# Kernel tuning notes

Measured on AMD Instinct MI355X. Metric: run time of the kernel, lower is better.

The kernel has to match this reference:

```python
import jax, jax.numpy as jnp
import numpy as np

B, T, D, H, N = 16, 512, 256, 4, 10
DK = D // H
EPS = 1e-12  # espnet LayerNorm eps


def _pe(t, d):
    # espnet PositionalEncoding table
    pos = np.arange(t, dtype=np.float32)[:, None]
    div = np.exp(np.arange(0, d, 2, dtype=np.float32) * (-np.log(10000.0) / d))
    pe = np.zeros((t, d), dtype=np.float32)
    pe[:, 0::2] = np.sin(pos * div)
    pe[:, 1::2] = np.cos(pos * div)
    return jnp.asarray(pe)


def _ln(x, g, b):
    m = jnp.mean(x, -1, keepdims=True)
    v = jnp.var(x, -1, keepdims=True)
    return (x - m) * jax.lax.rsqrt(v + EPS) * g + b


def _forward(x, x_lengths, lids, Wq, bq, Wk, bk, Wv, bv, Wo, bo, W1, b1, W2, b2, g1, be1, g2, be2, gf, bef):
    b, t, d = x.shape
    pe = _pe(t, d)
    pad = jnp.arange(t)[None, :] < x_lengths[:, None]          # [b,t] non-pad mask
    amask = pad[:, None, None, :]                               # [b,1,1,t] key mask
    onehot = (lids[:, None] == jnp.arange(N)[None, :]).astype(x.dtype)  # [b,N]
    h0 = x * np.float32(np.sqrt(d)) + pe[None]                  # scaled input + pos-enc (shared across experts)
    neg = jnp.finfo(x.dtype).min
    out = jnp.zeros_like(x)
    for z in range(N):  # fixed small set of structurally-distinct experts
        # pre-norm self-attention block
        hn = _ln(h0, g1[z], be1[z])
        q = (hn @ Wq[z] + bq[z]).reshape(b, t, H, DK).transpose(0, 2, 1, 3)
        k_ = (hn @ Wk[z] + bk[z]).reshape(b, t, H, DK).transpose(0, 2, 1, 3)
        v_ = (hn @ Wv[z] + bv[z]).reshape(b, t, H, DK).transpose(0, 2, 1, 3)
        scores = jnp.einsum('bhqd,bhkd->bhqk', q, k_) / np.float32(np.sqrt(DK))
        attn = jax.nn.softmax(jnp.where(amask, scores, neg), axis=-1)
        attn = jnp.where(amask, attn, jnp.zeros((), x.dtype))
        ctx = jnp.einsum('bhqk,bhkd->bhqd', attn, v_).transpose(0, 2, 1, 3).reshape(b, t, d)
        h = h0 + ctx @ Wo[z] + bo[z]
        # pre-norm feed-forward block
        hn2 = _ln(h, g2[z], be2[z])
        h = h + jax.nn.relu(hn2 @ W1[z] + b1[z]) @ W2[z] + b2[z]
        # final after_norm, then one-hot masked combine (== emb_lang sum)
        out = out + onehot[:, z, None, None] * _ln(h, gf[z], bef[z])
    return out


def setup_inputs() -> dict:
    key = jax.random.key(0)
    ks = jax.random.split(key, 12)
    s = np.float32(0.02)
    FF = 4 * D
    return {
        'x': jax.random.normal(ks[0], (B, T, D), jnp.float32),
        'x_lengths': jax.random.randint(ks[1], (B,), T // 2, T + 1),
        'lids': jax.random.randint(ks[2], (B,), 0, N),
        'Wq': jax.random.normal(ks[3], (N, D, D), jnp.float32) * s,
        'bq': jnp.zeros((N, D), jnp.float32),
        'Wk': jax.random.normal(ks[4], (N, D, D), jnp.float32) * s,
        'bk': jnp.zeros((N, D), jnp.float32),
        'Wv': jax.random.normal(ks[5], (N, D, D), jnp.float32) * s,
        'bv': jnp.zeros((N, D), jnp.float32),
        'Wo': jax.random.normal(ks[6], (N, D, D), jnp.float32) * s,
        'bo': jnp.zeros((N, D), jnp.float32),
        'W1': jax.random.normal(ks[7], (N, D, FF), jnp.float32) * s,
        'b1': jnp.zeros((N, FF), jnp.float32),
        'W2': jax.random.normal(ks[8], (N, FF, D), jnp.float32) * s,
        'b2': jnp.zeros((N, D), jnp.float32),
        'g1': jnp.ones((N, D), jnp.float32),
        'be1': jnp.zeros((N, D), jnp.float32),
        'g2': jnp.ones((N, D), jnp.float32),
        'be2': jnp.zeros((N, D), jnp.float32),
        'gf': jnp.ones((N, D), jnp.float32),
        'bef': jnp.zeros((N, D), jnp.float32),
    }


def reference(x, x_lengths, lids, Wq, bq, Wk, bk, Wv, bv, Wo, bo, W1, b1, W2, b2, g1, be1, g2, be2, gf, bef):
    return _forward(x, x_lengths, lids, Wq, bq, Wk, bk, Wv, bv, Wo, bo, W1, b1, W2, b2, g1, be1, g2, be2, gf, bef)
```

## Files before the change

### kernel.cpp

```cpp
#include <hip/hip_runtime.h>

typedef unsigned short u16;
typedef __bf16 bf16x8 __attribute__((ext_vector_type(8)));
typedef float  f32x4  __attribute__((ext_vector_type(4)));
typedef unsigned int   u32x4 __attribute__((ext_vector_type(4)));
typedef unsigned short u16x4 __attribute__((ext_vector_type(4)));

#define DEV __device__ __forceinline__

#define NB   16
#define TT   512
#define DD   256
#define HH   4
#define DKH  64
#define NLANG 10
#define FFD  1024

DEV u16 f2bf(float f) {
  unsigned int u = __builtin_bit_cast(unsigned int, f);
  return (u16)((u + 0x7fffu + ((u >> 16) & 1u)) >> 16);
}

DEV f32x4 zero4() { f32x4 z; z[0]=0.f; z[1]=0.f; z[2]=0.f; z[3]=0.f; return z; }

typedef __attribute__((address_space(1))) const unsigned int g_as1;
typedef __attribute__((address_space(3))) unsigned int l_as3;
DEV void load_lds16(const void* g, void* l) {
  __builtin_amdgcn_global_load_lds((g_as1*)g, (l_as3*)l, 16, 0, 0);
}

DEV bf16x8 lds_frag(const u16* lds, int row, int slot) {
  return *(const bf16x8*)(lds + row * 64 + ((slot ^ (row & 7)) << 3));
}

__global__ __launch_bounds__(256) void pre_kernel(
    const float* __restrict__ Wq, const float* __restrict__ Wk,
    const float* __restrict__ Wv, const float* __restrict__ Wo,
    const float* __restrict__ W1, const float* __restrict__ W2,
    u16* __restrict__ wtq, u16* __restrict__ wtk, u16* __restrict__ wtv,
    u16* __restrict__ wto, u16* __restrict__ wt1, u16* __restrict__ wt2,
    const float* __restrict__ x, float* __restrict__ h0, u16* __restrict__ hn,
    const float* __restrict__ g, const float* __restrict__ be,
    const int* __restrict__ lids) {
  __shared__ u16 tile[32][33];
  const int bx = blockIdx.x;
  if (bx < 7680) {
    const float* src; u16* dst; int R, C, z, r0, c0;
    if (bx < 2560) {
      const int w = bx / 640, rem = bx % 640;
      src = (w == 0) ? Wq : (w == 1) ? Wk : (w == 2) ? Wv : Wo;
      dst = (w == 0) ? wtq : (w == 1) ? wtk : (w == 2) ? wtv : wto;
      R = 256; C = 256; z = rem >> 6;
      const int rc = rem & 63; r0 = (rc >> 3) * 32; c0 = (rc & 7) * 32;
    } else if (bx < 5120) {
      const int rem = bx - 2560; src = W1; dst = wt1; R = 256; C = 1024;
      z = rem >> 8; const int rc = rem & 255; r0 = (rc >> 5) * 32; c0 = (rc & 31) * 32;
    } else {
      const int rem = bx - 5120; src = W2; dst = wt2; R = 1024; C = 256;
      z = rem >> 8; const int rc = rem & 255; r0 = (rc >> 3) * 32; c0 = (rc & 7) * 32;
    }
    bool used = false;
#pragma unroll
    for (int i = 0; i < NB; ++i) used |= (lids[i] == z);
    if (!used) return;
    const float* s = src + (size_t)z * R * C;
    u16* d = dst + (size_t)z * R * C;
    const int tx = threadIdx.x & 31, ty = threadIdx.x >> 5;
#pragma unroll
    for (int rr = 0; rr < 4; ++rr) {
      const int r = ty + rr * 8;
      tile[r][tx] = f2bf(s[(size_t)(r0 + r) * C + c0 + tx]);
    }
    __syncthreads();
#pragma unroll
    for (int rr = 0; rr < 4; ++rr) {
      const int cc = ty + rr * 8;
      d[(size_t)(c0 + cc) * R + r0 + tx] = tile[tx][cc];
    }
  } else {
    const int wave = threadIdx.x >> 6, lane = threadIdx.x & 63;
    const int row = (bx - 7680) * 4 + wave;
    const int b = row >> 9, t = row & 511;
    const int z = lids[b];
    const int c0 = lane * 4;
    const float4 xv = *(const float4*)(x + (size_t)row * DD + c0);
    const float kPE = -9.21034037197618f / 256.0f;
    float div0 = __expf(kPE * (float)c0);
    float div1 = __expf(kPE * (float)(c0 + 2));
    float a0 = div0 * (float)t, a1 = div1 * (float)t;
    float h[4];
    h[0] = xv.x * 16.0f + sinf(a0);
    h[1] = xv.y * 16.0f + cosf(a0);
    h[2] = xv.z * 16.0f + sinf(a1);
    h[3] = xv.w * 16.0f + cosf(a1);
    float s = h[0] + h[1] + h[2] + h[3];
    float ss = h[0]*h[0] + h[1]*h[1] + h[2]*h[2] + h[3]*h[3];
#pragma unroll
    for (int d = 1; d < 64; d <<= 1) { s += __shfl_xor(s, d); ss += __shfl_xor(ss, d); }
    float mean = s * (1.0f / 256.0f);
    float var  = ss * (1.0f / 256.0f) - mean * mean;
    float rstd = rsqrtf(var + 1e-12f);
    *(float4*)(h0 + (size_t)row * DD + c0) = make_float4(h[0], h[1], h[2], h[3]);
    u16x4 o;
#pragma unroll
    for (int j = 0; j < 4; ++j)
      o[j] = f2bf((h[j] - mean) * rstd * g[z * DD + c0 + j] + be[z * DD + c0 + j]);
    *(u16x4*)(hn + (size_t)row * DD + c0) = o;
  }
}

template<int OUTF32>
__global__ __launch_bounds__(256) void ln_kernel(const float* __restrict__ in,
                                                 void* __restrict__ outp,
                                                 const float* __restrict__ g,
                                                 const float* __restrict__ be,
                                                 const int* __restrict__ lids) {
  const int wave = threadIdx.x >> 6, lane = threadIdx.x & 63;
  const int row = blockIdx.x * 4 + wave;
  const int b = row >> 9;
  const int z = lids[b];
  const int c0 = lane * 4;
  const float4 v = *(const float4*)(in + (size_t)row * DD + c0);
  float h[4] = {v.x, v.y, v.z, v.w};
  float s = h[0] + h[1] + h[2] + h[3];
  float ss = h[0]*h[0] + h[1]*h[1] + h[2]*h[2] + h[3]*h[3];
#pragma unroll
  for (int d = 1; d < 64; d <<= 1) { s += __shfl_xor(s, d); ss += __shfl_xor(ss, d); }
  float mean = s * (1.0f / 256.0f);
  float var  = ss * (1.0f / 256.0f) - mean * mean;
  float rstd = rsqrtf(var + 1e-12f);
  if (OUTF32) {
    float4 o;
    o.x = (h[0] - mean) * rstd * g[z * DD + c0 + 0] + be[z * DD + c0 + 0];
    o.y = (h[1] - mean) * rstd * g[z * DD + c0 + 1] + be[z * DD + c0 + 1];
    o.z = (h[2] - mean) * rstd * g[z * DD + c0 + 2] + be[z * DD + c0 + 2];
    o.w = (h[3] - mean) * rstd * g[z * DD + c0 + 3] + be[z * DD + c0 + 3];
    *(float4*)((float*)outp + (size_t)row * DD + c0) = o;
  } else {
    u16x4 o;
#pragma unroll
    for (int j = 0; j < 4; ++j)
      o[j] = f2bf((h[j] - mean) * rstd * g[z * DD + c0 + j] + be[z * DD + c0 + j]);
    *(u16x4*)((u16*)outp + (size_t)row * DD + c0) = o;
  }
}

DEV void gemm_tile(const u16* __restrict__ A, const u16* __restrict__ W, int K,
                   int m0, int n0, u16* Alds, u16* Blds, f32x4 acc[4][4]) {
  const int tid = threadIdx.x;
  const int lane = tid & 63;
  const int wave = tid >> 6;
  const int wm = wave >> 1, wn = wave & 1;
  const int l15 = lane & 15, lhi = lane >> 4;
  const int lr = lane >> 3, lsl = lane & 7;
  const u16* srcA[4]; const u16* srcB[4];
#pragma unroll
  for (int j = 0; j < 4; ++j) {
    const int r = wave * 32 + j * 8 + lr;
    srcA[j] = A + (size_t)(m0 + r) * K + ((lsl ^ (r & 7)) << 3);
    srcB[j] = W + (size_t)(n0 + r) * K + ((lsl ^ (r & 7)) << 3);
  }
  for (int k0 = 0; k0 < K; k0 += 64) {
#pragma unroll
    for (int j = 0; j < 4; ++j) {
      load_lds16(srcA[j] + k0, Alds + (wave * 32 + j * 8) * 64);
      load_lds16(srcB[j] + k0, Blds + (wave * 32 + j * 8) * 64);
    }
    __syncthreads();
#pragma unroll
    for (int ks = 0; ks < 2; ++ks) {
      const int slot = ks * 4 + lhi;
      bf16x8 af[4], bfr[4];
#pragma unroll
      for (int m = 0; m < 4; ++m)
        af[m] = lds_frag(Alds, wm * 64 + m * 16 + l15, slot);
#pragma unroll
      for (int n = 0; n < 4; ++n)
        bfr[n] = lds_frag(Blds, wn * 64 + n * 16 + l15, slot);
#pragma unroll
      for (int m = 0; m < 4; ++m)
#pragma unroll
        for (int n = 0; n < 4; ++n)
          acc[m][n] = __builtin_amdgcn_mfma_f32_16x16x32_bf16(af[m], bfr[n], acc[m][n], 0, 0, 0);
    }
    __syncthreads();
  }
}

template<int EPI>
__global__ __launch_bounds__(256) void gemm_kernel(const u16* __restrict__ A,
                                                   const u16* __restrict__ Wt,
                                                   const float* __restrict__ bias,
                                                   const float* __restrict__ res,
                                                   void* __restrict__ outp,
                                                   const int* __restrict__ lids,
                                                   int N, int K) {
  __shared__ u16 Alds[128 * 64];
  __shared__ u16 Blds[128 * 64];
  const int b = blockIdx.z;
  const int z = lids[b];
  const int m0 = blockIdx.y * 128, n0 = blockIdx.x * 128;
  f32x4 acc[4][4];
#pragma unroll
  for (int i = 0; i < 4; ++i)
#pragma unroll
    for (int j = 0; j < 4; ++j) acc[i][j] = zero4();
  gemm_tile(A + (size_t)b * TT * K, Wt + (size_t)z * N * K, K, m0, n0, Alds, Blds, acc);
  const int lane = threadIdx.x & 63, wave = threadIdx.x >> 6;
  const int wm = wave >> 1, wn = wave & 1;
  const int l15 = lane & 15, lhi = lane >> 4;
  float bvv[4];
#pragma unroll
  for (int n = 0; n < 4; ++n) bvv[n] = bias[(size_t)z * N + n0 + wn * 64 + n * 16 + l15];
#pragma unroll
  for (int m = 0; m < 4; ++m) {
    const int grow = m0 + wm * 64 + m * 16 + lhi * 4;
#pragma unroll
    for (int n = 0; n < 4; ++n) {
      const int gcol = n0 + wn * 64 + n * 16 + l15;
#pragma unroll
      for (int r = 0; r < 4; ++r) {
        float v = acc[m][n][r] + bvv[n];
        size_t idx = (size_t)b * TT * N + (size_t)(grow + r) * N + gcol;
        if (EPI == 1) ((u16*)outp)[idx] = f2bf(v > 0.f ? v : 0.f);
        else ((u16*)outp)[idx] = f2bf(v);
      }
    }
  }
}

__global__ __launch_bounds__(256) void gemm64_kernel(const u16* __restrict__ A,
                                                     const u16* __restrict__ Wt,
                                                     const float* __restrict__ bias,
                                                     const float* __restrict__ res,
                                                     float* __restrict__ outp,
                                                     const int* __restrict__ lids,
                                                     int N, int K) {
  __shared__ u16 Alds[128 * 64];
  __shared__ u16 Blds[64 * 64];
  const int b = blockIdx.z;
  const int z = lids[b];
  const int m0 = blockIdx.y * 128, n0 = blockIdx.x * 64;
  const int tid = threadIdx.x, lane = tid & 63, wave = tid >> 6;
  const int l15 = lane & 15, lhi = lane >> 4;
  const int lr = lane >> 3, lsl = lane & 7;
  const u16* Ab = A + (size_t)b * TT * K;
  const u16* Wb = Wt + (size_t)z * N * K;
  const u16* srcA[4]; const u16* srcB[2];
#pragma unroll
  for (int j = 0; j < 4; ++j) {
    const int r = wave * 32 + j * 8 + lr;
    srcA[j] = Ab + (size_t)(m0 + r) * K + ((lsl ^ (r & 7)) << 3);
  }
#pragma unroll
  for (int j = 0; j < 2; ++j) {
    const int r = wave * 16 + j * 8 + lr;
    srcB[j] = Wb + (size_t)(n0 + r) * K + ((lsl ^ (r & 7)) << 3);
  }
  f32x4 acc[2][4];
#pragma unroll
  for (int i = 0; i < 2; ++i)
#pragma unroll
    for (int j = 0; j < 4; ++j) acc[i][j] = zero4();
  for (int k0 = 0; k0 < K; k0 += 64) {
#pragma unroll
    for (int j = 0; j < 4; ++j)
      load_lds16(srcA[j] + k0, Alds + (wave * 32 + j * 8) * 64);
#pragma unroll
    for (int j = 0; j < 2; ++j)
      load_lds16(srcB[j] + k0, Blds + (wave * 16 + j * 8) * 64);
    __syncthreads();
#pragma unroll
    for (int ks = 0; ks < 2; ++ks) {
      const int slot = ks * 4 + lhi;
      bf16x8 af[2], bfr[4];
#pragma unroll
      for (int m = 0; m < 2; ++m)
        af[m] = lds_frag(Alds, wave * 32 + m * 16 + l15, slot);
#pragma unroll
      for (int n = 0; n < 4; ++n)
        bfr[n] = lds_frag(Blds, n * 16 + l15, slot);
#pragma unroll
      for (int m = 0; m < 2; ++m)
#pragma unroll
        for (int n = 0; n < 4; ++n)
          acc[m][n] = __builtin_amdgcn_mfma_f32_16x16x32_bf16(af[m], bfr[n], acc[m][n], 0, 0, 0);
    }
    __syncthreads();
  }
  float bvv[4];
#pragma unroll
  for (int n = 0; n < 4; ++n) bvv[n] = bias[(size_t)z * N + n0 + n * 16 + l15];
#pragma unroll
  for (int m = 0; m < 2; ++m) {
    const int grow = m0 + wave * 32 + m * 16 + lhi * 4;
#pragma unroll
    for (int n = 0; n < 4; ++n) {
      const int gcol = n0 + n * 16 + l15;
#pragma unroll
      for (int r = 0; r < 4; ++r) {
        size_t idx = (size_t)b * TT * N + (size_t)(grow + r) * N + gcol;
        outp[idx] = res[idx] + acc[m][n][r] + bvv[n];
      }
    }
  }
}

__global__ __launch_bounds__(256) void gemm_qkv(const u16* __restrict__ A,
                                                const u16* __restrict__ wtq,
                                                const u16* __restrict__ wtk,
                                                const u16* __restrict__ wtv,
                                                const float* __restrict__ bq,
                                                const float* __restrict__ bk,
                                                const float* __restrict__ bv,
                                                u16* __restrict__ qo,
                                                u16* __restrict__ ko,
                                                u16* __restrict__ vto,
                                                const int* __restrict__ lids) {
  __shared__ u16 Alds[128 * 64];
  __shared__ u16 Blds[128 * 64];
  const int b = blockIdx.z & 15, which = blockIdx.z >> 4;
  const int z = lids[b];
  const u16* W = (which == 0) ? wtq : (which == 1) ? wtk : wtv;
  const float* bias = (which == 0) ? bq : (which == 1) ? bk : bv;
  const int m0 = blockIdx.y * 128, n0 = blockIdx.x * 128;
  f32x4 acc[4][4];
#pragma unroll
  for (int i = 0; i < 4; ++i)
#pragma unroll
    for (int j = 0; j < 4; ++j) acc[i][j] = zero4();
  gemm_tile(A + (size_t)b * TT * DD, W + (size_t)z * DD * DD, DD, m0, n0, Alds, Blds, acc);
  const int lane = threadIdx.x & 63, wave = threadIdx.x >> 6;
  const int wm = wave >> 1, wn = wave & 1;
  const int l15 = lane & 15, lhi = lane >> 4;
  float bvv[4];
#pragma unroll
  for (int n = 0; n < 4; ++n) bvv[n] = bias[(size_t)z * DD + n0 + wn * 64 + n * 16 + l15];
  if (which < 2) {
    u16* out = (which == 0) ? qo : ko;
#pragma unroll
    for (int m = 0; m < 4; ++m) {
      const int grow = m0 + wm * 64 + m * 16 + lhi * 4;
#pragma unroll
      for (int n = 0; n < 4; ++n) {
        const int gcol = n0 + wn * 64 + n * 16 + l15;
#pragma unroll
        for (int r = 0; r < 4; ++r)
          out[(size_t)b * TT * DD + (size_t)(grow + r) * DD + gcol] = f2bf(acc[m][n][r] + bvv[n]);
      }
    }
  } else {
#pragma unroll
    for (int m = 0; m < 4; ++m) {
      const int grow = m0 + wm * 64 + m * 16 + lhi * 4;
#pragma unroll
      for (int n = 0; n < 4; ++n) {
        const int gcol = n0 + wn * 64 + n * 16 + l15;
        u16x4 pk;
#pragma unroll
        for (int r = 0; r < 4; ++r) pk[r] = f2bf(acc[m][n][r] + bvv[n]);
        *(u16x4*)(vto + (size_t)(b * HH + (gcol >> 6)) * DKH * TT + (size_t)(gcol & 63) * TT + grow) = pk;
      }
    }
  }
}

__global__ __launch_bounds__(512, 4) void attn_kernel(const u16* __restrict__ q,
                                                      const u16* __restrict__ k,
                                                      const u16* __restrict__ vt,
                                                      u16* __restrict__ ctx,
                                                      const int* __restrict__ lens) {
  __shared__ char smem[65536];
  u16* Kbuf = (u16*)smem;
  u16* Pbuf = (u16*)(smem + 32768);
  float* Of = (float*)smem;
  float* Ml = (float*)(smem + 32768);
  float* Ll = (float*)(smem + 32768 + 256);

  const int qt = blockIdx.x, h = blockIdx.y, b = blockIdx.z;
  const int tid = threadIdx.x;
  const int lane = tid & 63, wave = tid >> 6;
  const int grp = wave >> 2, wq = wave & 3;
  const int l15 = lane & 15, lhi = lane >> 4;
  const int len = lens[b];
  const int nt = (len + 127) >> 7;
  const int iters = (nt + 1) >> 1;
  const int qrow0 = qt * 64 + wq * 16;
  const u16* qb = q + (size_t)b * TT * DD + h * DKH;
  const u16* kb = k + (size_t)b * TT * DD + h * DKH;
  const u16* vtb = vt + (size_t)(b * HH + h) * DKH * TT;
  const float SC = 0.125f * 1.4426950408889634f;

  u16* Kg = Kbuf + grp * (128 * 64);
  u16* Pg = Pbuf + grp * (64 * 128);

  bf16x8 qf[2];
#pragma unroll
  for (int ks = 0; ks < 2; ++ks)
    qf[ks] = *(const bf16x8*)(qb + (size_t)(qrow0 + l15) * DD + ks * 32 + lhi * 8);

  auto stage = [&](int t) {
    const int r0w = wq * 32;
#pragma unroll
    for (int j = 0; j < 4; ++j) {
      const int rb = r0w + j * 8;
      const int r = rb + (lane >> 3);
      const int s = (lane & 7) ^ (r & 7);
      load_lds16(kb + (size_t)(t * 128 + r) * DD + s * 8, Kg + rb * 64);
    }
  };

  float m[4] = {-1e30f, -1e30f, -1e30f, -1e30f};
  float l[4] = {0.f, 0.f, 0.f, 0.f};
  f32x4 o[4];
#pragma unroll
  for (int d0 = 0; d0 < 4; ++d0) o[d0] = zero4();

  stage(grp);

  for (int i = 0; i < iters; ++i) {
    __syncthreads();
    const int t = 2 * i + grp;
    const bool active = (t < nt);
    if (active) {
      f32x4 S[8];
#pragma unroll
      for (int nb = 0; nb < 8; ++nb) {
        f32x4 a = zero4();
#pragma unroll
        for (int ks = 0; ks < 2; ++ks) {
          const int row = nb * 16 + l15;
          const int swz = (ks * 64 + lhi * 16) ^ ((row & 7) << 4);
          bf16x8 kf = *(const bf16x8*)(Kg + row * 64 + (swz >> 1));
          a = __builtin_amdgcn_mfma_f32_16x16x32_bf16(qf[ks], kf, a, 0, 0, 0);
        }
        S[nb] = a;
      }
      float tmax[4] = {-1e30f, -1e30f, -1e30f, -1e30f};
#pragma unroll
      for (int nb = 0; nb < 8; ++nb) {
        const int col = t * 128 + nb * 16 + l15;
#pragma unroll
        for (int r = 0; r < 4; ++r) {
          float v = S[nb][r] * SC;
          v = (col < len) ? v : -1e30f;
          S[nb][r] = v;
          tmax[r] = fmaxf(tmax[r], v);
        }
      }
#pragma unroll
      for (int d = 1; d < 16; d <<= 1)
#pragma unroll
        for (int r = 0; r < 4; ++r) tmax[r] = fmaxf(tmax[r], __shfl_xor(tmax[r], d));
      float al[4];
#pragma unroll
      for (int r = 0; r < 4; ++r) {
        float mn = fmaxf(m[r], tmax[r]);
        al[r] = exp2f(m[r] - mn);
        m[r] = mn;
      }
      float rs[4] = {0.f, 0.f, 0.f, 0.f};
#pragma unroll
      for (int nb = 0; nb < 8; ++nb) {
#pragma unroll
        for (int r = 0; r < 4; ++r) {
          float p = exp2f(S[nb][r] - m[r]);
          rs[r] += p;
          const int lrow = wq * 16 + lhi * 4 + r;
          const int swzb = ((nb * 16 + l15) * 2) ^ ((lrow & 7) << 4);
          Pg[(lrow * 256 + swzb) >> 1] = f2bf(p);
        }
      }
#pragma unroll
      for (int d = 1; d < 16; d <<= 1)
#pragma unroll
        for (int r = 0; r < 4; ++r) rs[r] += __shfl_xor(rs[r], d);
#pragma unroll
      for (int r = 0; r < 4; ++r) l[r] = l[r] * al[r] + rs[r];
#pragma unroll
      for (int d0 = 0; d0 < 4; ++d0)
#pragma unroll
        for (int r = 0; r < 4; ++r) o[d0][r] *= al[r];
    }
    __syncthreads();
    if (t + 2 < nt) stage(t + 2);
    if (active) {
      const int arow = wq * 16 + l15;
#pragma unroll
      for (int ks = 0; ks < 4; ++ks) {
        const int swz = (ks * 64 + lhi * 16) ^ ((arow & 7) << 4);
        bf16x8 pf = *(const bf16x8*)(Pg + arow * 128 + (swz >> 1));
#pragma unroll
        for (int d0 = 0; d0 < 4; ++d0) {
          bf16x8 vf = *(const bf16x8*)(vtb + (size_t)(d0 * 16 + l15) * TT + t * 128 + ks * 32 + lhi * 8);
          o[d0] = __builtin_amdgcn_mfma_f32_16x16x32_bf16(pf, vf, o[d0], 0, 0, 0);
        }
      }
    }
  }

  __syncthreads();
  if (grp == 1) {
#pragma unroll
    for (int d0 = 0; d0 < 4; ++d0)
#pragma unroll
      for (int r = 0; r < 4; ++r)
        Of[(wq * 16 + lhi * 4 + r) * 68 + d0 * 16 + l15] = o[d0][r];
    if (l15 == 0) {
#pragma unroll
      for (int r = 0; r < 4; ++r) {
        Ml[wq * 16 + lhi * 4 + r] = m[r];
        Ll[wq * 16 + lhi * 4 + r] = l[r];
      }
    }
  }
  __syncthreads();
  if (grp == 0) {
    u16* cb = ctx + (size_t)b * TT * DD + h * DKH;
#pragma unroll
    for (int r = 0; r < 4; ++r) {
      const int lrow = wq * 16 + lhi * 4 + r;
      const float m1 = Ml[lrow], l1 = Ll[lrow];
      const float mn = fmaxf(m[r], m1);
      const float a0 = exp2f(m[r] - mn), a1 = exp2f(m1 - mn);
      const float linv = 1.0f / (l[r] * a0 + l1 * a1);
#pragma unroll
      for (int d0 = 0; d0 < 4; ++d0) {
        const float of = Of[lrow * 68 + d0 * 16 + l15];
        const float out = (o[d0][r] * a0 + of * a1) * linv;
        cb[(size_t)(qt * 64 + lrow) * DD + d0 * 16 + l15] = f2bf(out);
      }
    }
  }
}

extern "C" void kernel_launch(void* const* d_in, const int* in_sizes, int n_in,
                              void* d_out, int out_size, void* d_ws, size_t ws_size,
                              hipStream_t stream) {
  (void)in_sizes; (void)n_in; (void)out_size; (void)ws_size;
  const float* x    = (const float*)d_in[0];
  const int*   xlen = (const int*)d_in[1];
  const int*   lids = (const int*)d_in[2];
  const float* Wq = (const float*)d_in[3];
  const float* bq = (const float*)d_in[4];
  const float* Wk = (const float*)d_in[5];
  const float* bk = (const float*)d_in[6];
  const float* Wv = (const float*)d_in[7];
  const float* bv = (const float*)d_in[8];
  const float* Wo = (const float*)d_in[9];
  const float* bo = (const float*)d_in[10];
  const float* W1 = (const float*)d_in[11];
  const float* b1 = (const float*)d_in[12];
  const float* W2 = (const float*)d_in[13];
  const float* b2 = (const float*)d_in[14];
  const float* g1 = (const float*)d_in[15];
  const float* be1= (const float*)d_in[16];
  const float* g2 = (const float*)d_in[17];
  const float* be2= (const float*)d_in[18];
  const float* gf = (const float*)d_in[19];
  const float* bef= (const float*)d_in[20];

  char* ws = (char*)d_ws;
  size_t off = 0;
  auto alloc = [&](size_t bytes) -> void* {
    void* p = ws + off;
    off = (off + bytes + 255) & ~(size_t)255;
    return p;
  };
  u16* wtq = (u16*)alloc((size_t)NLANG * DD * DD * 2);
  u16* wtk = (u16*)alloc((size_t)NLANG * DD * DD * 2);
  u16* wtv = (u16*)alloc((size_t)NLANG * DD * DD * 2);
  u16* wto = (u16*)alloc((size_t)NLANG * DD * DD * 2);
  u16* wt1 = (u16*)alloc((size_t)NLANG * DD * FFD * 2);
  u16* wt2 = (u16*)alloc((size_t)NLANG * FFD * DD * 2);
  float* h0 = (float*)alloc((size_t)NB * TT * DD * 4);
  float* hc = (float*)alloc((size_t)NB * TT * DD * 4);
  u16* hn  = (u16*)alloc((size_t)NB * TT * DD * 2);
  u16* qb  = (u16*)alloc((size_t)NB * TT * DD * 2);
  u16* kb  = (u16*)alloc((size_t)NB * TT * DD * 2);
  u16* vtb = (u16*)alloc((size_t)NB * TT * DD * 2);
  u16* ctx = (u16*)alloc((size_t)NB * TT * DD * 2);
  u16* ffn = (u16*)alloc((size_t)NB * TT * FFD * 2);

  pre_kernel<<<dim3(7680 + 2048), 256, 0, stream>>>(
      Wq, Wk, Wv, Wo, W1, W2, wtq, wtk, wtv, wto, wt1, wt2,
      x, h0, hn, g1, be1, lids);

  gemm_qkv<<<dim3(2, 4, 48), 256, 0, stream>>>(hn, wtq, wtk, wtv, bq, bk, bv, qb, kb, vtb, lids);

  attn_kernel<<<dim3(8, HH, NB), 512, 0, stream>>>(qb, kb, vtb, ctx, xlen);

  gemm64_kernel<<<dim3(4, 4, NB), 256, 0, stream>>>(ctx, wto, bo, h0, hc, lids, DD, DD);

  ln_kernel<0><<<dim3(NB * TT / 4), 256, 0, stream>>>(hc, hn, g2, be2, lids);

  gemm_kernel<1><<<dim3(8, 4, NB), 256, 0, stream>>>(hn, wt1, b1, nullptr, ffn, lids, FFD, DD);

  gemm64_kernel<<<dim3(4, 4, NB), 256, 0, stream>>>(ffn, wt2, b2, hc, hc, lids, DD, FFD);

  ln_kernel<1><<<dim3(NB * TT / 4), 256, 0, stream>>>(hc, d_out, gf, bef, lids);
}
```

Baseline: 105.2 us.

## Fuse residual-add and LayerNorm into full-row GEMMs; drop K staging in attention

The Wo and W2 projections now run in a new gemm_ln_kernel. Each block computes all 256 output columns for 32 rows, so it can add bias and residual and apply LayerNorm in the epilogue. This removes two standalone LN kernels and a round trip of the fp32 hidden state through memory. The attention kernel drops its LDS double-buffered K staging and block-wide syncs and reads K fragments straight from global memory, with a per-wave P buffer and a flattened grid. In exchange the fused GEMM has only 256 blocks, each reloading the full weight slab, and the K loads in attention are now uncoalesced global reads.

```diff
diff --git a/kernel.cpp b/kernel.cpp
--- a/kernel.cpp
+++ b/kernel.cpp
@@ -109,42 +109,6 @@
   }
 }
 
-template<int OUTF32>
-__global__ __launch_bounds__(256) void ln_kernel(const float* __restrict__ in,
-                                                 void* __restrict__ outp,
-                                                 const float* __restrict__ g,
-                                                 const float* __restrict__ be,
-                                                 const int* __restrict__ lids) {
-  const int wave = threadIdx.x >> 6, lane = threadIdx.x & 63;
-  const int row = blockIdx.x * 4 + wave;
-  const int b = row >> 9;
-  const int z = lids[b];
-  const int c0 = lane * 4;
-  const float4 v = *(const float4*)(in + (size_t)row * DD + c0);
-  float h[4] = {v.x, v.y, v.z, v.w};
-  float s = h[0] + h[1] + h[2] + h[3];
-  float ss = h[0]*h[0] + h[1]*h[1] + h[2]*h[2] + h[3]*h[3];
-#pragma unroll
-  for (int d = 1; d < 64; d <<= 1) { s += __shfl_xor(s, d); ss += __shfl_xor(ss, d); }
-  float mean = s * (1.0f / 256.0f);
-  float var  = ss * (1.0f / 256.0f) - mean * mean;
-  float rstd = rsqrtf(var + 1e-12f);
-  if (OUTF32) {
-    float4 o;
-    o.x = (h[0] - mean) * rstd * g[z * DD + c0 + 0] + be[z * DD + c0 + 0];
-    o.y = (h[1] - mean) * rstd * g[z * DD + c0 + 1] + be[z * DD + c0 + 1];
-    o.z = (h[2] - mean) * rstd * g[z * DD + c0 + 2] + be[z * DD + c0 + 2];
-    o.w = (h[3] - mean) * rstd * g[z * DD + c0 + 3] + be[z * DD + c0 + 3];
-    *(float4*)((float*)outp + (size_t)row * DD + c0) = o;
-  } else {
-    u16x4 o;
-#pragma unroll
-    for (int j = 0; j < 4; ++j)
-      o[j] = f2bf((h[j] - mean) * rstd * g[z * DD + c0 + j] + be[z * DD + c0 + j]);
-    *(u16x4*)((u16*)outp + (size_t)row * DD + c0) = o;
-  }
-}
-
 DEV void gemm_tile(const u16* __restrict__ A, const u16* __restrict__ W, int K,
                    int m0, int n0, u16* Alds, u16* Blds, f32x4 acc[4][4]) {
   const int tid = threadIdx.x;
@@ -191,7 +155,6 @@
 __global__ __launch_bounds__(256) void gemm_kernel(const u16* __restrict__ A,
                                                    const u16* __restrict__ Wt,
                                                    const float* __restrict__ bias,
-                                                   const float* __restrict__ res,
                                                    void* __restrict__ outp,
                                                    const int* __restrict__ lids,
                                                    int N, int K) {
@@ -224,83 +187,6 @@
         size_t idx = (size_t)b * TT * N + (size_t)(grow + r) * N + gcol;
         if (EPI == 1) ((u16*)outp)[idx] = f2bf(v > 0.f ? v : 0.f);
         else ((u16*)outp)[idx] = f2bf(v);
-      }
-    }
-  }
-}
-
-__global__ __launch_bounds__(256) void gemm64_kernel(const u16* __restrict__ A,
-                                                     const u16* __restrict__ Wt,
-                                                     const float* __restrict__ bias,
-                                                     const float* __restrict__ res,
-                                                     float* __restrict__ outp,
-                                                     const int* __restrict__ lids,
-                                                     int N, int K) {
-  __shared__ u16 Alds[128 * 64];
-  __shared__ u16 Blds[64 * 64];
-  const int b = blockIdx.z;
-  const int z = lids[b];
-  const int m0 = blockIdx.y * 128, n0 = blockIdx.x * 64;
-  const int tid = threadIdx.x, lane = tid & 63, wave = tid >> 6;
-  const int l15 = lane & 15, lhi = lane >> 4;
-  const int lr = lane >> 3, lsl = lane & 7;
-  const u16* Ab = A + (size_t)b * TT * K;
-  const u16* Wb = Wt + (size_t)z * N * K;
-  const u16* srcA[4]; const u16* srcB[2];
-#pragma unroll
-  for (int j = 0; j < 4; ++j) {
-    const int r = wave * 32 + j * 8 + lr;
-    srcA[j] = Ab + (size_t)(m0 + r) * K + ((lsl ^ (r & 7)) << 3);
-  }
-#pragma unroll
-  for (int j = 0; j < 2; ++j) {
-    const int r = wave * 16 + j * 8 + lr;
-    srcB[j] = Wb + (size_t)(n0 + r) * K + ((lsl ^ (r & 7)) << 3);
-  }
-  f32x4 acc[2][4];
-#pragma unroll
-  for (int i = 0; i < 2; ++i)
-#pragma unroll
-    for (int j = 0; j < 4; ++j) acc[i][j] = zero4();
-  for (int k0 = 0; k0 < K; k0 += 64) {
-#pragma unroll
-    for (int j = 0; j < 4; ++j)
-      load_lds16(srcA[j] + k0, Alds + (wave * 32 + j * 8) * 64);
-#pragma unroll
-    for (int j = 0; j < 2; ++j)
-      load_lds16(srcB[j] + k0, Blds + (wave * 16 + j * 8) * 64);
-    __syncthreads();
-#pragma unroll
-    for (int ks = 0; ks < 2; ++ks) {
-      const int slot = ks * 4 + lhi;
-      bf16x8 af[2], bfr[4];
-#pragma unroll
-      for (int m = 0; m < 2; ++m)
-        af[m] = lds_frag(Alds, wave * 32 + m * 16 + l15, slot);
-#pragma unroll
-      for (int n = 0; n < 4; ++n)
-        bfr[n] = lds_frag(Blds, n * 16 + l15, slot);
-#pragma unroll
-      for (int m = 0; m < 2; ++m)
-#pragma unroll
-        for (int n = 0; n < 4; ++n)
-          acc[m][n] = __builtin_amdgcn_mfma_f32_16x16x32_bf16(af[m], bfr[n], acc[m][n], 0, 0, 0);
-    }
-    __syncthreads();
-  }
-  float bvv[4];
-#pragma unroll
-  for (int n = 0; n < 4; ++n) bvv[n] = bias[(size_t)z * N + n0 + n * 16 + l15];
-#pragma unroll
-  for (int m = 0; m < 2; ++m) {
-    const int grow = m0 + wave * 32 + m * 16 + lhi * 4;
-#pragma unroll
-    for (int n = 0; n < 4; ++n) {
-      const int gcol = n0 + n * 16 + l15;
-#pragma unroll
-      for (int r = 0; r < 4; ++r) {
-        size_t idx = (size_t)b * TT * N + (size_t)(grow + r) * N + gcol;
-        outp[idx] = res[idx] + acc[m][n][r] + bvv[n];
       }
     }
   }
@@ -370,45 +256,30 @@
                                                       const u16* __restrict__ vt,
                                                       u16* __restrict__ ctx,
                                                       const int* __restrict__ lens) {
-  __shared__ char smem[65536];
-  u16* Kbuf = (u16*)smem;
-  u16* Pbuf = (u16*)(smem + 32768);
-  float* Of = (float*)smem;
-  float* Ml = (float*)(smem + 32768);
-  float* Ll = (float*)(smem + 32768 + 256);
-
-  const int qt = blockIdx.x, h = blockIdx.y, b = blockIdx.z;
+  __shared__ char smem[33792];
+  const int id = blockIdx.x;
+  const int qt = id >> 6, bh = id & 63, b = bh >> 2, h = bh & 3;
   const int tid = threadIdx.x;
   const int lane = tid & 63, wave = tid >> 6;
   const int grp = wave >> 2, wq = wave & 3;
   const int l15 = lane & 15, lhi = lane >> 4;
   const int len = lens[b];
   const int nt = (len + 127) >> 7;
-  const int iters = (nt + 1) >> 1;
   const int qrow0 = qt * 64 + wq * 16;
   const u16* qb = q + (size_t)b * TT * DD + h * DKH;
   const u16* kb = k + (size_t)b * TT * DD + h * DKH;
   const u16* vtb = vt + (size_t)(b * HH + h) * DKH * TT;
   const float SC = 0.125f * 1.4426950408889634f;
 
-  u16* Kg = Kbuf + grp * (128 * 64);
-  u16* Pg = Pbuf + grp * (64 * 128);
+  u16* Pg = (u16*)(smem + wave * 4096);
+  float* Of = (float*)smem;
+  float* Ml = (float*)(smem + 32768);
+  float* Ll = (float*)(smem + 33024);
 
   bf16x8 qf[2];
 #pragma unroll
   for (int ks = 0; ks < 2; ++ks)
     qf[ks] = *(const bf16x8*)(qb + (size_t)(qrow0 + l15) * DD + ks * 32 + lhi * 8);
-
-  auto stage = [&](int t) {
-    const int r0w = wq * 32;
-#pragma unroll
-    for (int j = 0; j < 4; ++j) {
-      const int rb = r0w + j * 8;
-      const int r = rb + (lane >> 3);
-      const int s = (lane & 7) ^ (r & 7);
-      load_lds16(kb + (size_t)(t * 128 + r) * DD + s * 8, Kg + rb * 64);
-    }
-  };
 
   float m[4] = {-1e30f, -1e30f, -1e30f, -1e30f};
   float l[4] = {0.f, 0.f, 0.f, 0.f};
@@ -416,85 +287,71 @@
 #pragma unroll
   for (int d0 = 0; d0 < 4; ++d0) o[d0] = zero4();
 
-  stage(grp);
-
-  for (int i = 0; i < iters; ++i) {
-    __syncthreads();
-    const int t = 2 * i + grp;
-    const bool active = (t < nt);
-    if (active) {
-      f32x4 S[8];
-#pragma unroll
-      for (int nb = 0; nb < 8; ++nb) {
-        f32x4 a = zero4();
-#pragma unroll
-        for (int ks = 0; ks < 2; ++ks) {
-          const int row = nb * 16 + l15;
-          const int swz = (ks * 64 + lhi * 16) ^ ((row & 7) << 4);
-          bf16x8 kf = *(const bf16x8*)(Kg + row * 64 + (swz >> 1));
-          a = __builtin_amdgcn_mfma_f32_16x16x32_bf16(qf[ks], kf, a, 0, 0, 0);
-        }
-        S[nb] = a;
-      }
-      float tmax[4] = {-1e30f, -1e30f, -1e30f, -1e30f};
-#pragma unroll
-      for (int nb = 0; nb < 8; ++nb) {
-        const int col = t * 128 + nb * 16 + l15;
-#pragma unroll
-        for (int r = 0; r < 4; ++r) {
-          float v = S[nb][r] * SC;
-          v = (col < len) ? v : -1e30f;
-          S[nb][r] = v;
-          tmax[r] = fmaxf(tmax[r], v);
-        }
-      }
-#pragma unroll
-      for (int d = 1; d < 16; d <<= 1)
-#pragma unroll
-        for (int r = 0; r < 4; ++r) tmax[r] = fmaxf(tmax[r], __shfl_xor(tmax[r], d));
-      float al[4];
+  for (int t = grp; t < nt; t += 2) {
+    f32x4 S[8];
+#pragma unroll
+    for (int nb = 0; nb < 8; ++nb) {
+      f32x4 a = zero4();
+#pragma unroll
+      for (int ks = 0; ks < 2; ++ks) {
+        bf16x8 kf = *(const bf16x8*)(kb + (size_t)(t * 128 + nb * 16 + l15) * DD + ks * 32 + lhi * 8);
+        a = __builtin_amdgcn_mfma_f32_16x16x32_bf16(qf[ks], kf, a, 0, 0, 0);
+      }
+      S[nb] = a;
+    }
+    float tmax[4] = {-1e30f, -1e30f, -1e30f, -1e30f};
+#pragma unroll
+    for (int nb = 0; nb < 8; ++nb) {
+      const int col = t * 128 + nb * 16 + l15;
 #pragma unroll
       for (int r = 0; r < 4; ++r) {
-        float mn = fmaxf(m[r], tmax[r]);
-        al[r] = exp2f(m[r] - mn);
-        m[r] = mn;
-      }
-      float rs[4] = {0.f, 0.f, 0.f, 0.f};
-#pragma unroll
-      for (int nb = 0; nb < 8; ++nb) {
-#pragma unroll
-        for (int r = 0; r < 4; ++r) {
-          float p = exp2f(S[nb][r] - m[r]);
-          rs[r] += p;
-          const int lrow = wq * 16 + lhi * 4 + r;
-          const int swzb = ((nb * 16 + l15) * 2) ^ ((lrow & 7) << 4);
-          Pg[(lrow * 256 + swzb) >> 1] = f2bf(p);
-        }
-      }
-#pragma unroll
-      for (int d = 1; d < 16; d <<= 1)
-#pragma unroll
-        for (int r = 0; r < 4; ++r) rs[r] += __shfl_xor(rs[r], d);
-#pragma unroll
-      for (int r = 0; r < 4; ++r) l[r] = l[r] * al[r] + rs[r];
-#pragma unroll
-      for (int d0 = 0; d0 < 4; ++d0)
-#pragma unroll
-        for (int r = 0; r < 4; ++r) o[d0][r] *= al[r];
-    }
-    __syncthreads();
-    if (t + 2 < nt) stage(t + 2);
-    if (active) {
-      const int arow = wq * 16 + l15;
-#pragma unroll
-      for (int ks = 0; ks < 4; ++ks) {
-        const int swz = (ks * 64 + lhi * 16) ^ ((arow & 7) << 4);
-        bf16x8 pf = *(const bf16x8*)(Pg + arow * 128 + (swz >> 1));
-#pragma unroll
-        for (int d0 = 0; d0 < 4; ++d0) {
-          bf16x8 vf = *(const bf16x8*)(vtb + (size_t)(d0 * 16 + l15) * TT + t * 128 + ks * 32 + lhi * 8);
-          o[d0] = __builtin_amdgcn_mfma_f32_16x16x32_bf16(pf, vf, o[d0], 0, 0, 0);
-        }
+        float v = S[nb][r] * SC;
+        v = (col < len) ? v : -1e30f;
+        S[nb][r] = v;
+        tmax[r] = fmaxf(tmax[r], v);
+      }
+    }
+#pragma unroll
+    for (int d = 1; d < 16; d <<= 1)
+#pragma unroll
+      for (int r = 0; r < 4; ++r) tmax[r] = fmaxf(tmax[r], __shfl_xor(tmax[r], d));
+    float al[4];
+#pragma unroll
+    for (int r = 0; r < 4; ++r) {
+      float mn = fmaxf(m[r], tmax[r]);
+      al[r] = exp2f(m[r] - mn);
+      m[r] = mn;
+    }
+    float rs[4] = {0.f, 0.f, 0.f, 0.f};
+#pragma unroll
+    for (int nb = 0; nb < 8; ++nb) {
+#pragma unroll
+      for (int r = 0; r < 4; ++r) {
+        float p = exp2f(S[nb][r] - m[r]);
+        rs[r] += p;
+        const int row16 = lhi * 4 + r;
+        const int swzb = ((nb * 16 + l15) * 2) ^ ((row16 & 7) << 4);
+        Pg[(row16 * 256 + swzb) >> 1] = f2bf(p);
+      }
+    }
+#pragma unroll
+    for (int d = 1; d < 16; d <<= 1)
+#pragma unroll
+      for (int r = 0; r < 4; ++r) rs[r] += __shfl_xor(rs[r], d);
+#pragma unroll
+    for (int r = 0; r < 4; ++r) l[r] = l[r] * al[r] + rs[r];
+#pragma unroll
+    for (int d0 = 0; d0 < 4; ++d0)
+#pragma unroll
+      for (int r = 0; r < 4; ++r) o[d0][r] *= al[r];
+#pragma unroll
+    for (int ks = 0; ks < 4; ++ks) {
+      const int swz = (ks * 64 + lhi * 16) ^ ((l15 & 7) << 4);
+      bf16x8 pf = *(const bf16x8*)(Pg + ((l15 * 256 + swz) >> 1));
+#pragma unroll
+      for (int d0 = 0; d0 < 4; ++d0) {
+        bf16x8 vf = *(const bf16x8*)(vtb + (size_t)(d0 * 16 + l15) * TT + t * 128 + ks * 32 + lhi * 8);
+        o[d0] = __builtin_amdgcn_mfma_f32_16x16x32_bf16(pf, vf, o[d0], 0, 0, 0);
       }
     }
   }
@@ -529,6 +386,122 @@
         const float of = Of[lrow * 68 + d0 * 16 + l15];
         const float out = (o[d0][r] * a0 + of * a1) * linv;
         cb[(size_t)(qt * 64 + lrow) * DD + d0 * 16 + l15] = f2bf(out);
+      }
+    }
+  }
+}
+
+template<int FINAL>
+__global__ __launch_bounds__(512) void gemm_ln_kernel(
+    const u16* __restrict__ A, const u16* __restrict__ Wt,
+    const float* __restrict__ bias, const float* __restrict__ res,
+    float* __restrict__ outf, u16* __restrict__ outbf,
+    const float* __restrict__ g, const float* __restrict__ be,
+    const int* __restrict__ lids, int K) {
+  __shared__ u16 Alds[32 * 64];
+  __shared__ u16 Blds[256 * 64];
+  __shared__ float Sred[2][4][16];
+  __shared__ float SSred[2][4][16];
+  const int b = blockIdx.y;
+  const int z = lids[b];
+  const int m0 = blockIdx.x * 32;
+  const int tid = threadIdx.x, lane = tid & 63, wave = tid >> 6;
+  const int l15 = lane & 15, lhi = lane >> 4;
+  const int lr = lane >> 3, lsl = lane & 7;
+  const u16* Ab = A + (size_t)b * TT * K;
+  const u16* Wb = Wt + (size_t)z * 256 * K;
+  const u16* srcA = Ab;
+  if (wave < 4) {
+    const int rA = wave * 8 + lr;
+    srcA = Ab + (size_t)(m0 + rA) * K + ((lsl ^ (rA & 7)) << 3);
+  }
+  const u16* srcB[4];
+#pragma unroll
+  for (int j = 0; j < 4; ++j) {
+    const int rB = wave * 32 + j * 8 + lr;
+    srcB[j] = Wb + (size_t)rB * K + ((lsl ^ (rB & 7)) << 3);
+  }
+  f32x4 acc[4];
+#pragma unroll
+  for (int n = 0; n < 4; ++n) acc[n] = zero4();
+  for (int k0 = 0; k0 < K; k0 += 64) {
+    if (wave < 4) load_lds16(srcA + k0, Alds + (wave * 8) * 64);
+#pragma unroll
+    for (int j = 0; j < 4; ++j)
+      load_lds16(srcB[j] + k0, Blds + (wave * 32 + j * 8) * 64);
+    __syncthreads();
+#pragma unroll
+    for (int ks = 0; ks < 2; ++ks) {
+      const int slot = ks * 4 + lhi;
+      bf16x8 af = lds_frag(Alds, (wave >> 2) * 16 + l15, slot);
+#pragma unroll
+      for (int n = 0; n < 4; ++n) {
+        bf16x8 bf = lds_frag(Blds, (wave & 3) * 64 + n * 16 + l15, slot);
+        acc[n] = __builtin_amdgcn_mfma_f32_16x16x32_bf16(af, bf, acc[n], 0, 0, 0);
+      }
+    }
+    __syncthreads();
+  }
+  const int rbase = m0 + (wave >> 2) * 16;
+  const int cq = (wave & 3) * 64;
+  float bv[4], gv[4], bev[4];
+#pragma unroll
+  for (int n = 0; n < 4; ++n) {
+    const int col = cq + n * 16 + l15;
+    bv[n]  = bias[(size_t)z * 256 + col];
+    gv[n]  = g[(size_t)z * 256 + col];
+    bev[n] = be[(size_t)z * 256 + col];
+  }
+  float v[4][4];
+  float sr[4] = {0.f, 0.f, 0.f, 0.f}, ssr[4] = {0.f, 0.f, 0.f, 0.f};
+#pragma unroll
+  for (int n = 0; n < 4; ++n) {
+#pragma unroll
+    for (int r = 0; r < 4; ++r) {
+      const size_t idx = ((size_t)b * TT + rbase + lhi * 4 + r) * 256 + cq + n * 16 + l15;
+      float t = acc[n][r] + bv[n] + res[idx];
+      v[n][r] = t;
+      sr[r] += t;
+      ssr[r] += t * t;
+    }
+  }
+#pragma unroll
+  for (int d = 1; d < 16; d <<= 1)
+#pragma unroll
+    for (int r = 0; r < 4; ++r) { sr[r] += __shfl_xor(sr[r], d); ssr[r] += __shfl_xor(ssr[r], d); }
+  if (l15 == 0) {
+#pragma unroll
+    for (int r = 0; r < 4; ++r) {
+      Sred[wave >> 2][wave & 3][lhi * 4 + r] = sr[r];
+      SSred[wave >> 2][wave & 3][lhi * 4 + r] = ssr[r];
+    }
+  }
+  __syncthreads();
+  float meanr[4], rstdr[4];
+#pragma unroll
+  for (int r = 0; r < 4; ++r) {
+    float tot = 0.f, tss = 0.f;
+#pragma unroll
+    for (int qd = 0; qd < 4; ++qd) {
+      tot += Sred[wave >> 2][qd][lhi * 4 + r];
+      tss += SSred[wave >> 2][qd][lhi * 4 + r];
+    }
+    const float mean = tot * (1.0f / 256.0f);
+    const float var  = tss * (1.0f / 256.0f) - mean * mean;
+    meanr[r] = mean;
+    rstdr[r] = rsqrtf(var + 1e-12f);
+  }
+#pragma unroll
+  for (int n = 0; n < 4; ++n) {
+#pragma unroll
+    for (int r = 0; r < 4; ++r) {
+      const size_t idx = ((size_t)b * TT + rbase + lhi * 4 + r) * 256 + cq + n * 16 + l15;
+      const float ln = (v[n][r] - meanr[r]) * rstdr[r] * gv[n] + bev[n];
+      if (FINAL) {
+        outf[idx] = ln;
+      } else {
+        outf[idx] = v[n][r];
+        outbf[idx] = f2bf(ln);
       }
     }
   }
@@ -588,15 +561,11 @@
 
   gemm_qkv<<<dim3(2, 4, 48), 256, 0, stream>>>(hn, wtq, wtk, wtv, bq, bk, bv, qb, kb, vtb, lids);
 
-  attn_kernel<<<dim3(8, HH, NB), 512, 0, stream>>>(qb, kb, vtb, ctx, xlen);
-
-  gemm64_kernel<<<dim3(4, 4, NB), 256, 0, stream>>>(ctx, wto, bo, h0, hc, lids, DD, DD);
-
-  ln_kernel<0><<<dim3(NB * TT / 4), 256, 0, stream>>>(hc, hn, g2, be2, lids);
-
-  gemm_kernel<1><<<dim3(8, 4, NB), 256, 0, stream>>>(hn, wt1, b1, nullptr, ffn, lids, FFD, DD);
-
-  gemm64_kernel<<<dim3(4, 4, NB), 256, 0, stream>>>(ffn, wt2, b2, hc, hc, lids, DD, FFD);
-
-  ln_kernel<1><<<dim3(NB * TT / 4), 256, 0, stream>>>(hc, d_out, gf, bef, lids);
-}
+  attn_kernel<<<dim3(512), 512, 0, stream>>>(qb, kb, vtb, ctx, xlen);
+
+  gemm_ln_kernel<0><<<dim3(16, NB), 512, 0, stream>>>(ctx, wto, bo, h0, hc, hn, g2, be2, lids, DD);
+
+  gemm_kernel<1><<<dim3(8, 4, NB), 256, 0, stream>>>(hn, wt1, b1, ffn, lids, FFD, DD);
+
+  gemm_ln_kernel<1><<<dim3(16, NB), 512, 0, stream>>>(ffn, wt2, b2, hc, (float*)d_out, nullptr, gf, bef, lids, FFD);
+}
```

Measured after the change: 105.7 us. Within noise of the previous version (+0.4%).
